# Optimization experiments

Hardware: AMD Instinct MI355X
Metric: run time of the kernel (lower is better)

Reference implementation:

```python
import jax, jax.numpy as jnp
import numpy as np
import math

PHI = (1.0 + math.sqrt(5.0)) / 2.0
LN_EPS = 1e-5


def _carrier_phases(n_heads: int) -> np.ndarray:
    """Reproduce DimensionalHeadManager._allocate carrier phases."""
    base = [k * math.pi / 7.0 for k in range(7)]  # rung base phases
    n_rungs = 7
    raw = []
    remaining = n_heads
    for i in range(n_rungs):
        if i < n_rungs - 1:
            c = max(1, round(n_heads / PHI ** (i + 1)))
            c = min(c, remaining - (n_rungs - 1 - i))
            raw.append(c)
            remaining -= c
        else:
            raw.append(max(1, remaining))
    phases = []
    for rung_idx, count in enumerate(raw):
        for j in range(count):
            phases.append(base[rung_idx] + 2.0 * math.pi / max(count, 1) * j)
    return np.asarray(phases[:n_heads], dtype=np.float32)


def setup_inputs() -> dict:
    key = jax.random.key(0)
    ks = jax.random.split(key, 7)
    B, S, D, H = 2, 2048, 1024, 16
    w_scale = 0.02  # realistic init scale for Linear weights
    x = jax.random.normal(ks[0], (B, S, D), dtype=jnp.float32)
    Wq = jax.random.normal(ks[1], (D, D), dtype=jnp.float32) * w_scale
    Wk = jax.random.normal(ks[2], (D, D), dtype=jnp.float32) * w_scale
    Wv = jax.random.normal(ks[3], (D, D), dtype=jnp.float32) * w_scale
    Wo = jax.random.normal(ks[4], (D, D), dtype=jnp.float32) * w_scale
    Wp = jax.random.normal(ks[5], (D,), dtype=jnp.float32) * w_scale  # W_phase (1,D) flattened
    gamma = jnp.ones((D,), dtype=jnp.float32)
    beta = jnp.zeros((D,), dtype=jnp.float32)
    carrier = jnp.asarray(_carrier_phases(H))  # srl.carrier_freq init
    lam = jnp.float32(0.1)  # lambda_resonance init
    return {"x": x, "Wq": Wq, "Wk": Wk, "Wv": Wv, "Wo": Wo, "Wp": Wp,
            "gamma": gamma, "beta": beta, "carrier": carrier, "lam": lam}


def reference(x, Wq, Wk, Wv, Wo, Wp, gamma, beta, carrier, lam):
    B, S, D = x.shape
    H = carrier.shape[0]
    dh = D // H
    scale = 1.0 / math.sqrt(dh)

    residual = x
    # LayerNorm
    mu = jnp.mean(x, axis=-1, keepdims=True)
    var = jnp.mean((x - mu) ** 2, axis=-1, keepdims=True)
    xn = (x - mu) * jax.lax.rsqrt(var + LN_EPS) * gamma + beta

    # Q/K/V projections (torch Linear: y = x @ W.T), split into heads
    q = jnp.einsum('bsd,ed->bse', xn, Wq).reshape(B, S, H, dh)
    k = jnp.einsum('bsd,ed->bse', xn, Wk).reshape(B, S, H, dh)
    v = jnp.einsum('bsd,ed->bse', xn, Wv).reshape(B, S, H, dh)

    # scalar phase per token, per-head carrier resonance gate
    phase = jnp.einsum('bsd,d->bs', xn, Wp)                       # (B,S)
    head_T = jnp.cos((phase[..., None] - carrier) * 0.5) ** 2     # (B,S,H)

    # attention scores + resonance term R_ij = cos^2((phi_i - phi_j)/2)
    scores = jnp.einsum('bihd,bjhd->bhij', q, k) * scale          # (B,H,S,S)
    R = jnp.cos((phase[:, :, None] - phase[:, None, :]) * 0.5) ** 2  # (B,S,S)
    scores = scores + lam * R[:, None, :, :]

    attn = jax.nn.softmax(scores, axis=-1)
    out = jnp.einsum('bhij,bjhd->bihd', attn, v)                  # (B,S,H,dh)
    out = out * head_T[..., None]                                 # per-head resonance gating
    emergent_energy = jnp.sum(jnp.abs(out))
    y = residual + jnp.einsum('bse,de->bsd', out.reshape(B, S, D), Wo)
    return (y, emergent_energy)
```

## Files before the change

kernel.cpp:

```cpp
#include <hip/hip_runtime.h>
#include <hip/hip_bf16.h>

#define S_LEN 2048
#define D_MODEL 1024
#define NH 16
#define DH 64
#define M_TOK 4096
#define DK 80

typedef __attribute__((ext_vector_type(8))) short bf16x8;
typedef __attribute__((ext_vector_type(4))) float f32x4;
typedef __attribute__((ext_vector_type(16))) float f32x16;

#define LOG2E 1.4426950408889634f

__device__ __forceinline__ unsigned short f2bf(float f) {
  unsigned u = __float_as_uint(f);
  u += 0x7FFF + ((u >> 16) & 1);
  return (unsigned short)(u >> 16);
}

__device__ __forceinline__ void gl16(const void* g, void* l) {
  __builtin_amdgcn_global_load_lds(
      (const __attribute__((address_space(1))) unsigned int*)g,
      (__attribute__((address_space(3))) unsigned int*)l, 16, 0, 0);
}

__device__ __forceinline__ void pl32swap(unsigned int& a, unsigned int& b) {
  asm volatile("v_permlane32_swap_b32 %0, %1" : "+v"(a), "+v"(b));
}

__global__ __launch_bounds__(256) void prep_kernel(
    const float* __restrict__ Wq, const float* __restrict__ Wk,
    const float* __restrict__ Wv, const float* __restrict__ Wo,
    unsigned short* __restrict__ wbf, float* __restrict__ energy) {
  if (blockIdx.x == 0 && threadIdx.x == 0) *energy = 0.f;
  int idx = (blockIdx.x * 256 + threadIdx.x) * 4;
  int wsel = idx >> 20;
  const float* s = (wsel == 0) ? Wq : (wsel == 1) ? Wk : (wsel == 2) ? Wv : Wo;
  int off = idx & 1048575;
  float4 v = *(const float4*)(s + off);
  ushort4 p;
  p.x = f2bf(v.x); p.y = f2bf(v.y); p.z = f2bf(v.z); p.w = f2bf(v.w);
  *(ushort4*)(wbf + idx) = p;
}

__device__ __forceinline__ float block_sum(float v, float* sm) {
#pragma unroll
  for (int o = 32; o > 0; o >>= 1) v += __shfl_xor(v, o, 64);
  int w = threadIdx.x >> 6;
  __syncthreads();
  if ((threadIdx.x & 63) == 0) sm[w] = v;
  __syncthreads();
  return sm[0] + sm[1] + sm[2] + sm[3];
}

__global__ __launch_bounds__(256) void ln_phase_kernel(
    const float* __restrict__ x, const float* __restrict__ Wp,
    const float* __restrict__ gamma, const float* __restrict__ beta,
    unsigned short* __restrict__ xn, float* __restrict__ cosP,
    float* __restrict__ sinP) {
  __shared__ float sm[4];
  int row = blockIdx.x;
  int tid = threadIdx.x;
  float4 v = ((const float4*)(x + (size_t)row * D_MODEL))[tid];
  float mu = block_sum(v.x + v.y + v.z + v.w, sm) * (1.0f / D_MODEL);
  float d0 = v.x - mu, d1 = v.y - mu, d2 = v.z - mu, d3 = v.w - mu;
  float var = block_sum(d0 * d0 + d1 * d1 + d2 * d2 + d3 * d3, sm) * (1.0f / D_MODEL);
  float rinv = rsqrtf(var + 1e-5f);
  float4 g = ((const float4*)gamma)[tid];
  float4 be = ((const float4*)beta)[tid];
  float n0 = d0 * rinv * g.x + be.x;
  float n1 = d1 * rinv * g.y + be.y;
  float n2 = d2 * rinv * g.z + be.z;
  float n3 = d3 * rinv * g.w + be.w;
  ushort4 p;
  p.x = f2bf(n0); p.y = f2bf(n1); p.z = f2bf(n2); p.w = f2bf(n3);
  ((ushort4*)(xn + (size_t)row * D_MODEL))[tid] = p;
  float4 wp = ((const float4*)Wp)[tid];
  float ph = block_sum(n0 * wp.x + n1 * wp.y + n2 * wp.z + n3 * wp.w, sm);
  if (tid == 0) {
    cosP[row] = cosf(ph);
    sinP[row] = sinf(ph);
  }
}

__global__ __launch_bounds__(256) void phase_fill_kernel(
    const float* __restrict__ cosP, const float* __restrict__ sinP,
    unsigned short* __restrict__ kk80) {
  int gid = blockIdx.x * 256 + threadIdx.x;
  int s = gid & (S_LEN - 1);
  int bh = gid >> 11;
  int b = bh >> 4;
  int tok = b * S_LEN + s;
  unsigned int w0 = (unsigned int)f2bf(cosP[tok]) | ((unsigned int)f2bf(sinP[tok]) << 16);
  *(int4*)(kk80 + (size_t)gid * DK + 64) = make_int4((int)w0, 0, 0, 0);
}

__global__ __launch_bounds__(256, 3) void qkv_gemm_kernel(
    const unsigned short* __restrict__ xn, const unsigned short* __restrict__ wbf,
    unsigned short* __restrict__ q, unsigned short* __restrict__ kk80,
    unsigned short* __restrict__ vT) {
  __shared__ __align__(16) unsigned short As[128 * 64];
  __shared__ __align__(16) unsigned short Bs[128 * 64];
  int bid = blockIdx.x;
  bool vmode = bid >= 512;
  const unsigned short* Ap;
  const unsigned short* Bp;
  int m0, n0;
  if (!vmode) {
    m0 = (bid >> 4) * 128;
    n0 = (bid & 15) * 128;
    Ap = xn; Bp = wbf;
  } else {
    int v2 = bid - 512;
    m0 = (v2 & 7) * 128;
    n0 = (v2 >> 3) * 128;
    Ap = wbf + 2 * D_MODEL * D_MODEL; Bp = xn;
  }
  int tid = threadIdx.x;
  int wave = tid >> 6, lane = tid & 63, quad = lane >> 4, l15 = lane & 15;
  int wm = (wave & 1) * 64, wn = (wave >> 1) * 64;
  f32x4 acc[4][4];
#pragma unroll
  for (int r = 0; r < 4; ++r)
#pragma unroll
    for (int c = 0; c < 4; ++c) acc[r][c] = (f32x4){0.f, 0.f, 0.f, 0.f};

  for (int k0 = 0; k0 < D_MODEL; k0 += 64) {
    __syncthreads();
#pragma unroll
    for (int t = 0; t < 4; ++t) {
      int c = t * 256 + tid;
      int r = c >> 3, p = c & 7;
      int g = p ^ (r & 7);
      gl16(&Ap[(size_t)(m0 + r) * D_MODEL + k0 + g * 8], &As[c * 8]);
      gl16(&Bp[(size_t)(n0 + r) * D_MODEL + k0 + g * 8], &Bs[c * 8]);
    }
    __syncthreads();
    bf16x8 af[4][2], bfr[4][2];
#pragma unroll
    for (int r = 0; r < 4; ++r) {
      int R = wm + r * 16 + l15;
#pragma unroll
      for (int h = 0; h < 2; ++h)
        af[r][h] = *(const bf16x8*)&As[R * 64 + ((h * 4 + quad) ^ (R & 7)) * 8];
    }
#pragma unroll
    for (int c = 0; c < 4; ++c) {
      int R = wn + c * 16 + l15;
#pragma unroll
      for (int h = 0; h < 2; ++h)
        bfr[c][h] = *(const bf16x8*)&Bs[R * 64 + ((h * 4 + quad) ^ (R & 7)) * 8];
    }
#pragma unroll
    for (int h = 0; h < 2; ++h)
#pragma unroll
      for (int r = 0; r < 4; ++r)
#pragma unroll
        for (int c = 0; c < 4; ++c)
          acc[r][c] = __builtin_amdgcn_mfma_f32_16x16x32_bf16(af[r][h], bfr[c][h], acc[r][c], 0, 0, 0);
  }
#pragma unroll
  for (int r = 0; r < 4; ++r) {
#pragma unroll
    for (int c = 0; c < 4; ++c) {
#pragma unroll
      for (int rr = 0; rr < 4; ++rr) {
        if (vmode) {
          int e = m0 + wm + r * 16 + quad * 4 + rr;
          int tok = n0 + wn + c * 16 + l15;
          int hh = e >> 6, d = e & 63;
          int bb = tok >> 11, ss = tok & (S_LEN - 1);
          vT[(((size_t)(bb * NH + hh)) * DH + d) * S_LEN + ss] = f2bf(acc[r][c][rr]);
        } else {
          int tok = m0 + wm + r * 16 + quad * 4 + rr;
          int n = n0 + wn + c * 16 + l15;
          int e = n & 1023;
          int hh = e >> 6, d = e & 63;
          int bb = tok >> 11, ss = tok & (S_LEN - 1);
          if ((n0 >> 10) == 0) {
            q[(((size_t)(bb * NH + hh)) * S_LEN + ss) * DH + d] =
                f2bf(acc[r][c][rr] * (0.125f * LOG2E));
          } else {
            kk80[(((size_t)(bb * NH + hh)) * S_LEN + ss) * DK + d] = f2bf(acc[r][c][rr]);
          }
        }
      }
    }
  }
}

__global__ __launch_bounds__(128, 2) void attn_kernel(
    const unsigned short* __restrict__ q, const unsigned short* __restrict__ kk80,
    const unsigned short* __restrict__ vT, const float* __restrict__ cosP,
    const float* __restrict__ sinP, const float* __restrict__ carrier,
    const float* __restrict__ lamp, unsigned short* __restrict__ outw,
    float* __restrict__ energy) {
  __shared__ __align__(16) unsigned short Ks[2][64 * 72];
  __shared__ __align__(16) unsigned short Vs[2][512 * 8];
  __shared__ float Lr[2][32];
  __shared__ float er[2];
  int qt = blockIdx.x, h = blockIdx.y, b = blockIdx.z;
  int bh = b * NH + h;
  int tid = threadIdx.x, wave = tid >> 6, lane = tid & 63;
  int half = lane >> 5, l31 = lane & 31;

  const unsigned short* kb = kk80 + (size_t)bh * S_LEN * DK;
  const unsigned short* vb = vT + (size_t)bh * DH * S_LEN;
  int qrow = qt * 64 + wave * 32 + l31;

  bf16x8 bQ[5];
  {
    const unsigned short* qp = q + ((size_t)bh * S_LEN + qrow) * DH;
#pragma unroll
    for (int db = 0; db < 4; ++db)
      bQ[db] = *(const bf16x8*)(qp + db * 16 + half * 8);
    bf16x8 z8 = {0, 0, 0, 0, 0, 0, 0, 0};
    if (half == 0) {
      float hl2 = 0.5f * lamp[0] * LOG2E;
      z8[0] = (short)f2bf(hl2 * cosP[b * S_LEN + qrow]);
      z8[1] = (short)f2bf(hl2 * sinP[b * S_LEN + qrow]);
    }
    bQ[4] = z8;
  }

  f32x16 O0 = {}, O1 = {};
  float l_i = 0.f;

  auto stage = [&](int bi, int jbase) {
    unsigned short* ksd = &Ks[bi][0];
    unsigned short* vsd = &Vs[bi][0];
#pragma unroll
    for (int t = 0; t < 4; ++t) {
      unsigned int cc = t * 128 + tid;
      unsigned int r = cc / 9u, p = cc - r * 9u;
      gl16(&kb[(size_t)(jbase + r) * DK + p * 8], ksd + cc * 8);
    }
    if (tid < 64) {
      unsigned int cc = 512 + tid;
      unsigned int r = cc / 9u, p = cc - r * 9u;
      gl16(&kb[(size_t)(jbase + r) * DK + p * 8], ksd + cc * 8);
    }
#pragma unroll
    for (int t = 0; t < 4; ++t) {
      int cc = t * 128 + tid;
      int r = cc >> 3, p = cc & 7;
      int g = p ^ (r & 7);
      gl16(&vb[(size_t)r * S_LEN + jbase + g * 8], vsd + cc * 8);
    }
  };

  int cur = 0;
  stage(0, 0);
  __syncthreads();

  for (int jt = 0; jt < 32; ++jt) {
    if (jt < 31) stage(cur ^ 1, (jt + 1) * 64);

    const unsigned short* ksb = &Ks[cur][0];
    const unsigned short* vsb = &Vs[cur][0];

    f32x16 Sf[2];
#pragma unroll
    for (int sj = 0; sj < 2; ++sj) {
      Sf[sj] = (f32x16){};
      int r = sj * 32 + l31;
      __builtin_amdgcn_s_setprio(1);
#pragma unroll
      for (int db = 0; db < 5; ++db) {
        int p = (db < 4) ? (db * 2 + half) : 8;
        bf16x8 aK = *(const bf16x8*)(ksb + (r * 9 + p) * 8);
        Sf[sj] = __builtin_amdgcn_mfma_f32_32x32x16_bf16(aK, bQ[db], Sf[sj], 0, 0, 0);
      }
      __builtin_amdgcn_s_setprio(0);
    }

#pragma unroll
    for (int sj = 0; sj < 2; ++sj) {
      unsigned int w[8];
#pragma unroll
      for (int rr = 0; rr < 8; ++rr) {
        float e0 = exp2f(Sf[sj][rr * 2 + 0]);
        float e1 = exp2f(Sf[sj][rr * 2 + 1]);
        l_i += e0 + e1;
        __hip_bfloat162 pk2 = __float22bfloat162_rn(float2{e0, e1});
        w[rr] = *(unsigned int*)&pk2;
      }
#pragma unroll
      for (int u = 0; u < 2; ++u) {
        unsigned int a0 = w[u * 4 + 0], a1 = w[u * 4 + 1];
        unsigned int b0 = w[u * 4 + 2], b1 = w[u * 4 + 3];
        pl32swap(a0, b0);
        pl32swap(a1, b1);
        union { unsigned int u4[4]; bf16x8 v; } cvt;
        cvt.u4[0] = a0; cvt.u4[1] = a1; cvt.u4[2] = b0; cvt.u4[3] = b1;
        int jb = sj * 2 + u;
        __builtin_amdgcn_s_setprio(1);
        {
          int rv = l31;
          int p = (jb * 2 + half) ^ (rv & 7);
          bf16x8 bV = *(const bf16x8*)(vsb + (rv * 8 + p) * 8);
          O0 = __builtin_amdgcn_mfma_f32_32x32x16_bf16(cvt.v, bV, O0, 0, 0, 0);
        }
        {
          int rv = 32 + l31;
          int p = (jb * 2 + half) ^ (rv & 7);
          bf16x8 bV = *(const bf16x8*)(vsb + (rv * 8 + p) * 8);
          O1 = __builtin_amdgcn_mfma_f32_32x32x16_bf16(cvt.v, bV, O1, 0, 0, 0);
        }
        __builtin_amdgcn_s_setprio(0);
      }
    }

    __syncthreads();
    cur ^= 1;
  }

  l_i += __shfl_xor(l_i, 32, 64);
  Lr[wave][l31] = l_i;
  float ch = cosf(carrier[h]), sh = sinf(carrier[h]);
  float esum = 0.f;
#pragma unroll
  for (int reg = 0; reg < 16; ++reg) {
    int ir = (reg & 3) + 8 * (reg >> 2) + 4 * half;
    int srow = qt * 64 + wave * 32 + ir;
    float cp = cosP[b * S_LEN + srow], sp = sinP[b * S_LEN + srow];
    float gate = 0.5f + 0.5f * (cp * ch + sp * sh);
    float gl = gate / Lr[wave][ir];
    float v0 = O0[reg] * gl, v1 = O1[reg] * gl;
    esum += fabsf(v0) + fabsf(v1);
    size_t tok = (size_t)b * S_LEN + srow;
    outw[tok * D_MODEL + h * DH + l31] = f2bf(v0);
    outw[tok * D_MODEL + h * DH + 32 + l31] = f2bf(v1);
  }
#pragma unroll
  for (int off = 32; off > 0; off >>= 1) esum += __shfl_xor(esum, off, 64);
  if (lane == 0) er[wave] = esum;
  __syncthreads();
  if (tid == 0) atomicAdd(energy, er[0] + er[1]);
}

__global__ __launch_bounds__(256) void out_gemm_kernel(
    const unsigned short* __restrict__ A, const unsigned short* __restrict__ Wo,
    const float* __restrict__ x, float* __restrict__ y) {
  __shared__ __align__(16) unsigned short As[128 * 64];
  __shared__ __align__(16) unsigned short Bs[64 * 64];
  int tid = threadIdx.x;
  int wave = tid >> 6, lane = tid & 63, quad = lane >> 4, l15 = lane & 15;
  int wm = (wave & 1) * 64, wn = (wave >> 1) * 32;
  int m0 = blockIdx.y * 128, n0 = blockIdx.x * 64;
  f32x4 acc[4][2];
#pragma unroll
  for (int r = 0; r < 4; ++r)
#pragma unroll
    for (int c = 0; c < 2; ++c) acc[r][c] = (f32x4){0.f, 0.f, 0.f, 0.f};

  for (int k0 = 0; k0 < D_MODEL; k0 += 64) {
    __syncthreads();
#pragma unroll
    for (int t = 0; t < 4; ++t) {
      int c = t * 256 + tid;
      int r = c >> 3, p = c & 7;
      int qc = p ^ (r & 7);
      gl16(&A[(size_t)(m0 + r) * D_MODEL + k0 + qc * 8], &As[c * 8]);
    }
#pragma unroll
    for (int t = 0; t < 2; ++t) {
      int c = t * 256 + tid;
      int r = c >> 3, p = c & 7;
      int qc = p ^ (r & 7);
      gl16(&Wo[(size_t)(n0 + r) * D_MODEL + k0 + qc * 8], &Bs[c * 8]);
    }
    __syncthreads();
    bf16x8 af[4][2], bfr[2][2];
#pragma unroll
    for (int r = 0; r < 4; ++r) {
      int R = wm + r * 16 + l15;
#pragma unroll
      for (int h = 0; h < 2; ++h)
        af[r][h] = *(const bf16x8*)&As[R * 64 + ((h * 4 + quad) ^ (R & 7)) * 8];
    }
#pragma unroll
    for (int c = 0; c < 2; ++c) {
      int R = wn + c * 16 + l15;
#pragma unroll
      for (int h = 0; h < 2; ++h)
        bfr[c][h] = *(const bf16x8*)&Bs[R * 64 + ((h * 4 + quad) ^ (R & 7)) * 8];
    }
#pragma unroll
    for (int h = 0; h < 2; ++h)
#pragma unroll
      for (int r = 0; r < 4; ++r)
#pragma unroll
        for (int c = 0; c < 2; ++c)
          acc[r][c] = __builtin_amdgcn_mfma_f32_16x16x32_bf16(af[r][h], bfr[c][h], acc[r][c], 0, 0, 0);
  }
#pragma unroll
  for (int r = 0; r < 4; ++r) {
#pragma unroll
    for (int c = 0; c < 2; ++c) {
      int dcol = n0 + wn + c * 16 + l15;
#pragma unroll
      for (int rr = 0; rr < 4; ++rr) {
        int tok = m0 + wm + r * 16 + quad * 4 + rr;
        size_t idx = (size_t)tok * D_MODEL + dcol;
        y[idx] = x[idx] + acc[r][c][rr];
      }
    }
  }
}

extern "C" void kernel_launch(void* const* d_in, const int* in_sizes, int n_in,
                              void* d_out, int out_size, void* d_ws, size_t ws_size,
                              hipStream_t stream) {
  const float* x = (const float*)d_in[0];
  const float* Wq = (const float*)d_in[1];
  const float* Wk = (const float*)d_in[2];
  const float* Wv = (const float*)d_in[3];
  const float* Wo = (const float*)d_in[4];
  const float* Wp = (const float*)d_in[5];
  const float* gamma = (const float*)d_in[6];
  const float* beta = (const float*)d_in[7];
  const float* carrier = (const float*)d_in[8];
  const float* lam = (const float*)d_in[9];

  char* ws = (char*)d_ws;
  const size_t MB = 1024 * 1024;
  unsigned short* wbf = (unsigned short*)(ws);
  unsigned short* xn = (unsigned short*)(ws + 8 * MB);
  unsigned short* qq = (unsigned short*)(ws + 16 * MB);
  unsigned short* kk80 = (unsigned short*)(ws + 24 * MB);
  unsigned short* vT = (unsigned short*)(ws + 34 * MB);
  float* cosP = (float*)(ws + 42 * MB);
  float* sinP = (float*)(ws + 42 * MB + 16 * 1024);
  unsigned short* outw = xn;

  float* y = (float*)d_out;
  float* energy = y + (out_size - 1);

  prep_kernel<<<4096, 256, 0, stream>>>(Wq, Wk, Wv, Wo, wbf, energy);
  ln_phase_kernel<<<M_TOK, 256, 0, stream>>>(x, Wp, gamma, beta, xn, cosP, sinP);
  phase_fill_kernel<<<256, 256, 0, stream>>>(cosP, sinP, kk80);
  qkv_gemm_kernel<<<768, 256, 0, stream>>>(xn, wbf, qq, kk80, vT);
  attn_kernel<<<dim3(32, 16, 2), 128, 0, stream>>>(qq, kk80, vT, cosP, sinP,
                                                   carrier, lam, outw, energy);
  out_gemm_kernel<<<dim3(16, 32), 256, 0, stream>>>(outw, wbf + 3 * D_MODEL * D_MODEL,
                                                    x, y);
}
```

Baseline: 225.6 us.

## Split attention over key range with separate combine kernel

```diff
diff --git a/kernel.cpp b/kernel.cpp
--- a/kernel.cpp
+++ b/kernel.cpp
@@ -7,6 +7,7 @@
 #define DH 64
 #define M_TOK 4096
 #define DK 80
+#define JS 2
 
 typedef __attribute__((ext_vector_type(8))) short bf16x8;
 typedef __attribute__((ext_vector_type(4))) float f32x4;
@@ -191,17 +192,16 @@
   }
 }
 
-__global__ __launch_bounds__(128, 2) void attn_kernel(
+__global__ __launch_bounds__(128, 4) void attn_kernel(
     const unsigned short* __restrict__ q, const unsigned short* __restrict__ kk80,
     const unsigned short* __restrict__ vT, const float* __restrict__ cosP,
-    const float* __restrict__ sinP, const float* __restrict__ carrier,
-    const float* __restrict__ lamp, unsigned short* __restrict__ outw,
-    float* __restrict__ energy) {
-  __shared__ __align__(16) unsigned short Ks[2][64 * 72];
-  __shared__ __align__(16) unsigned short Vs[2][512 * 8];
-  __shared__ float Lr[2][32];
-  __shared__ float er[2];
-  int qt = blockIdx.x, h = blockIdx.y, b = blockIdx.z;
+    const float* __restrict__ sinP, const float* __restrict__ lamp,
+    float* __restrict__ Opart, float* __restrict__ lpart) {
+  __shared__ __align__(16) unsigned short Ks[64 * 72];
+  __shared__ __align__(16) unsigned short Vs[512 * 8];
+  int xx = blockIdx.x;
+  int qt = xx & 31, js = xx >> 5;
+  int h = blockIdx.y, b = blockIdx.z;
   int bh = b * NH + h;
   int tid = threadIdx.x, wave = tid >> 6, lane = tid & 63;
   int half = lane >> 5, l31 = lane & 31;
@@ -228,38 +228,28 @@
   f32x16 O0 = {}, O1 = {};
   float l_i = 0.f;
 
-  auto stage = [&](int bi, int jbase) {
-    unsigned short* ksd = &Ks[bi][0];
-    unsigned short* vsd = &Vs[bi][0];
+  for (int jt = 0; jt < S_LEN / (64 * JS); ++jt) {
+    int jbase = js * (S_LEN / JS) + jt * 64;
+    __syncthreads();
 #pragma unroll
     for (int t = 0; t < 4; ++t) {
       unsigned int cc = t * 128 + tid;
       unsigned int r = cc / 9u, p = cc - r * 9u;
-      gl16(&kb[(size_t)(jbase + r) * DK + p * 8], ksd + cc * 8);
+      gl16(&kb[(size_t)(jbase + r) * DK + p * 8], (unsigned short*)Ks + cc * 8);
     }
     if (tid < 64) {
       unsigned int cc = 512 + tid;
       unsigned int r = cc / 9u, p = cc - r * 9u;
-      gl16(&kb[(size_t)(jbase + r) * DK + p * 8], ksd + cc * 8);
+      gl16(&kb[(size_t)(jbase + r) * DK + p * 8], (unsigned short*)Ks + cc * 8);
     }
 #pragma unroll
     for (int t = 0; t < 4; ++t) {
       int cc = t * 128 + tid;
       int r = cc >> 3, p = cc & 7;
       int g = p ^ (r & 7);
-      gl16(&vb[(size_t)r * S_LEN + jbase + g * 8], vsd + cc * 8);
-    }
-  };
-
-  int cur = 0;
-  stage(0, 0);
-  __syncthreads();
-
-  for (int jt = 0; jt < 32; ++jt) {
-    if (jt < 31) stage(cur ^ 1, (jt + 1) * 64);
-
-    const unsigned short* ksb = &Ks[cur][0];
-    const unsigned short* vsb = &Vs[cur][0];
+      gl16(&vb[(size_t)r * S_LEN + jbase + g * 8], (unsigned short*)Vs + cc * 8);
+    }
+    __syncthreads();
 
     f32x16 Sf[2];
 #pragma unroll
@@ -270,7 +260,7 @@
 #pragma unroll
       for (int db = 0; db < 5; ++db) {
         int p = (db < 4) ? (db * 2 + half) : 8;
-        bf16x8 aK = *(const bf16x8*)(ksb + (r * 9 + p) * 8);
+        bf16x8 aK = *(const bf16x8*)((const unsigned short*)Ks + (r * 9 + p) * 8);
         Sf[sj] = __builtin_amdgcn_mfma_f32_32x32x16_bf16(aK, bQ[db], Sf[sj], 0, 0, 0);
       }
       __builtin_amdgcn_s_setprio(0);
@@ -300,45 +290,61 @@
         {
           int rv = l31;
           int p = (jb * 2 + half) ^ (rv & 7);
-          bf16x8 bV = *(const bf16x8*)(vsb + (rv * 8 + p) * 8);
+          bf16x8 bV = *(const bf16x8*)((const unsigned short*)Vs + (rv * 8 + p) * 8);
           O0 = __builtin_amdgcn_mfma_f32_32x32x16_bf16(cvt.v, bV, O0, 0, 0, 0);
         }
         {
           int rv = 32 + l31;
           int p = (jb * 2 + half) ^ (rv & 7);
-          bf16x8 bV = *(const bf16x8*)(vsb + (rv * 8 + p) * 8);
+          bf16x8 bV = *(const bf16x8*)((const unsigned short*)Vs + (rv * 8 + p) * 8);
           O1 = __builtin_amdgcn_mfma_f32_32x32x16_bf16(cvt.v, bV, O1, 0, 0, 0);
         }
         __builtin_amdgcn_s_setprio(0);
       }
     }
-
-    __syncthreads();
-    cur ^= 1;
   }
 
   l_i += __shfl_xor(l_i, 32, 64);
-  Lr[wave][l31] = l_i;
-  float ch = cosf(carrier[h]), sh = sinf(carrier[h]);
-  float esum = 0.f;
+  size_t obase = (size_t)(js * 2 * NH + bh) * S_LEN;
 #pragma unroll
   for (int reg = 0; reg < 16; ++reg) {
     int ir = (reg & 3) + 8 * (reg >> 2) + 4 * half;
     int srow = qt * 64 + wave * 32 + ir;
-    float cp = cosP[b * S_LEN + srow], sp = sinP[b * S_LEN + srow];
-    float gate = 0.5f + 0.5f * (cp * ch + sp * sh);
-    float gl = gate / Lr[wave][ir];
-    float v0 = O0[reg] * gl, v1 = O1[reg] * gl;
-    esum += fabsf(v0) + fabsf(v1);
-    size_t tok = (size_t)b * S_LEN + srow;
-    outw[tok * D_MODEL + h * DH + l31] = f2bf(v0);
-    outw[tok * D_MODEL + h * DH + 32 + l31] = f2bf(v1);
-  }
-#pragma unroll
-  for (int off = 32; off > 0; off >>= 1) esum += __shfl_xor(esum, off, 64);
-  if (lane == 0) er[wave] = esum;
-  __syncthreads();
-  if (tid == 0) atomicAdd(energy, er[0] + er[1]);
+    Opart[(obase + srow) * DH + l31] = O0[reg];
+    Opart[(obase + srow) * DH + 32 + l31] = O1[reg];
+  }
+  if (half == 0) lpart[obase + qt * 64 + wave * 32 + l31] = l_i;
+}
+
+__global__ __launch_bounds__(256) void combine_kernel(
+    const float* __restrict__ Opart, const float* __restrict__ lpart,
+    const float* __restrict__ cosP, const float* __restrict__ sinP,
+    const float* __restrict__ carrier, unsigned short* __restrict__ outw,
+    float* __restrict__ energy) {
+  __shared__ float sm[4];
+  int tok = blockIdx.x;
+  int b = tok >> 11, s = tok & (S_LEN - 1);
+  int t = threadIdx.x;
+  int c0 = t * 4;
+  int h = c0 >> 6, d0 = c0 & 63;
+  int bh = b * NH + h;
+  const size_t plane = (size_t)2 * NH * S_LEN;
+  size_t row0 = (size_t)bh * S_LEN + s;
+  float4 a0 = *(const float4*)(Opart + row0 * DH + d0);
+  float4 a1 = *(const float4*)(Opart + (plane + row0) * DH + d0);
+  float l = lpart[row0] + lpart[plane + row0];
+  float ch = cosf(carrier[h]), sh = sinf(carrier[h]);
+  float cp = cosP[tok], sp = sinP[tok];
+  float gate = 0.5f + 0.5f * (cp * ch + sp * sh);
+  float gl = gate / l;
+  float v0 = (a0.x + a1.x) * gl, v1 = (a0.y + a1.y) * gl;
+  float v2 = (a0.z + a1.z) * gl, v3 = (a0.w + a1.w) * gl;
+  ushort4 p;
+  p.x = f2bf(v0); p.y = f2bf(v1); p.z = f2bf(v2); p.w = f2bf(v3);
+  *(ushort4*)(outw + (size_t)tok * D_MODEL + c0) = p;
+  float esum = fabsf(v0) + fabsf(v1) + fabsf(v2) + fabsf(v3);
+  float tot = block_sum(esum, sm);
+  if (t == 0) atomicAdd(energy, tot);
 }
 
 __global__ __launch_bounds__(256) void out_gemm_kernel(
@@ -434,6 +440,8 @@
   unsigned short* vT = (unsigned short*)(ws + 34 * MB);
   float* cosP = (float*)(ws + 42 * MB);
   float* sinP = (float*)(ws + 42 * MB + 16 * 1024);
+  float* Opart = (float*)(ws + 43 * MB);
+  float* lpart = (float*)(ws + 75 * MB);
   unsigned short* outw = xn;
 
   float* y = (float*)d_out;
@@ -443,8 +451,10 @@
   ln_phase_kernel<<<M_TOK, 256, 0, stream>>>(x, Wp, gamma, beta, xn, cosP, sinP);
   phase_fill_kernel<<<256, 256, 0, stream>>>(cosP, sinP, kk80);
   qkv_gemm_kernel<<<768, 256, 0, stream>>>(xn, wbf, qq, kk80, vT);
-  attn_kernel<<<dim3(32, 16, 2), 128, 0, stream>>>(qq, kk80, vT, cosP, sinP,
-                                                   carrier, lam, outw, energy);
+  attn_kernel<<<dim3(32 * JS, 16, 2), 128, 0, stream>>>(qq, kk80, vT, cosP, sinP,
+                                                        lam, Opart, lpart);
+  combine_kernel<<<M_TOK, 256, 0, stream>>>(Opart, lpart, cosP, sinP, carrier,
+                                            outw, energy);
   out_gemm_kernel<<<dim3(16, 32), 256, 0, stream>>>(outw, wbf + 3 * D_MODEL * D_MODEL,
                                                     x, y);
 }
```

Result: slower. 288.7 us (+28.0%).
